# Performance work log

Measured on AMD Instinct MI355X. Metric: run time of the kernel, lower is better.

The kernel has to match this reference:

```python
import jax, jax.numpy as jnp
import numpy as np

N_DOMAINS = 8
LN_EPS = 1e-5


def setup_inputs() -> dict:
    key = jax.random.key(0)
    ks = jax.random.split(key, 4)
    N, D_IN, D_HID, D_OUT = 32768, 256, 1024, 256
    x = jax.random.normal(ks[0], (N, D_IN), dtype=jnp.float32)
    domain_types = jax.random.randint(ks[1], (N,), 0, N_DOMAINS, dtype=jnp.int32)
    # Per-domain MLP parameters (8 independent experts)
    W1 = jax.random.normal(ks[2], (N_DOMAINS, D_IN, D_HID), dtype=jnp.float32) * (1.0 / np.sqrt(D_IN))
    b1 = jnp.zeros((N_DOMAINS, D_HID), dtype=jnp.float32)
    gamma = jnp.ones((N_DOMAINS, D_HID), dtype=jnp.float32)
    beta = jnp.zeros((N_DOMAINS, D_HID), dtype=jnp.float32)
    W2 = jax.random.normal(ks[3], (N_DOMAINS, D_HID, D_OUT), dtype=jnp.float32) * (1.0 / np.sqrt(D_HID))
    b2 = jnp.zeros((N_DOMAINS, D_OUT), dtype=jnp.float32)
    return {"x": x, "domain_types": domain_types, "W1": W1, "b1": b1,
            "gamma": gamma, "beta": beta, "W2": W2, "b2": b2}


def _expert_mlp(x, W1d, b1d, gd, bd, W2d, b2d):
    # Linear -> LayerNorm -> ReLU -> (Dropout: identity at eval) -> Linear
    h = x @ W1d + b1d                       # [N, hid]
    mu = jnp.mean(h, axis=-1, keepdims=True)
    var = jnp.mean(jnp.square(h - mu), axis=-1, keepdims=True)
    h = (h - mu) * jax.lax.rsqrt(var + LN_EPS) * gd + bd
    h = jax.nn.relu(h)
    return h @ W2d + b2d                    # [N, out]


def reference(x, domain_types, W1, b1, gamma, beta, W2, b2):
    # output dim == x.shape[-1] (as in the torch code: zeros(batch, x.shape[-1]))
    out = jnp.zeros((x.shape[0], x.shape[-1]), dtype=x.dtype)
    for d in range(N_DOMAINS):  # small fixed expert loop (static MoE dispatch)
        y = _expert_mlp(x, W1[d], b1[d], gamma[d], beta[d], W2[d], b2[d])
        mask = (domain_types == d)[:, None]
        out = jnp.where(mask, y, out)
    return out
```

## Files before the change

kernel.cpp:

```cpp
#include <hip/hip_runtime.h>
#include <hip/hip_bf16.h>


#define ND 8
#define NROWS 32768
#define DIN 256
#define DHID 1024
#define DOUT 256
#define MPAD 33792
#define NTILES 264

typedef short short8 __attribute__((ext_vector_type(8)));
typedef unsigned short ushort8v __attribute__((ext_vector_type(8)));
typedef float floatx4 __attribute__((ext_vector_type(4)));

__device__ __forceinline__ unsigned short f2bf(float f) {
    unsigned u = __builtin_bit_cast(unsigned, f);
    unsigned r = u + 0x7fff + ((u >> 16) & 1);
    return (unsigned short)(r >> 16);
}
__device__ __forceinline__ float bf2f(unsigned short h) {
    unsigned u = ((unsigned)h) << 16;
    return __builtin_bit_cast(float, u);
}

#define GLDS16(gp, lp) __builtin_amdgcn_global_load_lds( \
    (const __attribute__((address_space(1))) void*)(gp), \
    (__attribute__((address_space(3))) void*)(lp), 16, 0, 0)

__global__ void transpose_histo(const float* __restrict__ W1,
                                const float* __restrict__ W2,
                                unsigned short* __restrict__ W1T,
                                unsigned short* __restrict__ W2T,
                                const int* __restrict__ dt,
                                int* __restrict__ counts) {
    const int z = blockIdx.z;
    if (z == 16) {
        const int bid = blockIdx.y * 8 + blockIdx.x;
        if (bid >= NROWS / 256) return;
        __shared__ int lc[ND];
        if (threadIdx.x < ND) lc[threadIdx.x] = 0;
        __syncthreads();
        atomicAdd(&lc[dt[bid * 256 + threadIdx.x]], 1);
        __syncthreads();
        if (threadIdx.x < ND) atomicAdd(&counts[threadIdx.x], lc[threadIdx.x]);
        return;
    }
    __shared__ float t[32][33];
    const bool isW1 = z < ND;
    const int d = isW1 ? z : z - ND;
    const int R = isW1 ? DIN : DHID;
    const int C = isW1 ? DHID : DOUT;
    const int r0 = (isW1 ? blockIdx.x : blockIdx.y) * 32;
    const int c0 = (isW1 ? blockIdx.y : blockIdx.x) * 32;
    const int tx = threadIdx.x & 31, ty = threadIdx.x >> 5;
    const float* src = (isW1 ? W1 : W2) + (size_t)d * R * C;
    unsigned short* dst = (isW1 ? W1T : W2T) + (size_t)d * R * C;
#pragma unroll
    for (int i = 0; i < 32; i += 8)
        t[ty + i][tx] = src[(size_t)(r0 + ty + i) * C + c0 + tx];
    __syncthreads();
#pragma unroll
    for (int i = 0; i < 32; i += 8)
        dst[(size_t)(c0 + ty + i) * R + r0 + tx] = f2bf(t[tx][ty + i]);
}

__global__ void make_meta(const int* __restrict__ counts, int* __restrict__ cursors,
                          int2* __restrict__ meta, int* __restrict__ perm) {
    __shared__ int ps[ND], pe[ND];
    if (threadIdx.x == 0) {
        int off = 0, t = 0;
        for (int d = 0; d < ND; d++) {
            cursors[d] = off;
            int nt = (counts[d] + 127) >> 7;
            for (int i = 0; i < nt; i++) meta[t++] = make_int2(d, off + (i << 7));
            ps[d] = off + counts[d];
            pe[d] = off + (nt << 7);
            off += nt << 7;
        }
        for (; t < NTILES; t++) meta[t] = make_int2(-1, 0);
    }
    __syncthreads();
#pragma unroll
    for (int d = 0; d < ND; d++)
        for (int p = ps[d] + threadIdx.x; p < pe[d]; p += 256) perm[p] = -1;
}

__global__ __launch_bounds__(256)
void assign_copy(const float* __restrict__ x, const int* __restrict__ dt,
                 int* __restrict__ cursors, int* __restrict__ perm,
                 unsigned short* __restrict__ xs) {
    __shared__ int lcnt[ND], lbase[ND];
    __shared__ int spos[256];
    const int tid = threadIdx.x;
    if (tid < ND) lcnt[tid] = 0;
    __syncthreads();
    const int r = blockIdx.x * 256 + tid;
    const int d = dt[r];
    const int myrank = atomicAdd(&lcnt[d], 1);
    __syncthreads();
    if (tid < ND && lcnt[tid] > 0)
        lbase[tid] = atomicAdd(&cursors[tid], lcnt[tid]);
    __syncthreads();
    const int p = lbase[d] + myrank;
    spos[tid] = p;
    perm[p] = r;
    __syncthreads();
    const int lane = tid & 63;
    const int sub = tid >> 6;
    for (int it = 0; it < 64; ++it) {
        const int lr = it * 4 + sub;
        const int gr = blockIdx.x * 256 + lr;
        const int pp = spos[lr];
        float4 v = ((const float4*)(x + (size_t)gr * DIN))[lane];
        ushort4 o;
        o.x = f2bf(v.x); o.y = f2bf(v.y); o.z = f2bf(v.z); o.w = f2bf(v.w);
        ((ushort4*)(xs + (size_t)pp * DIN))[lane] = o;
    }
}

__global__ __launch_bounds__(256, 2)
void gemm_a(const unsigned short* __restrict__ A,
            const unsigned short* __restrict__ Bt,
            const float* __restrict__ bias,
            const int2* __restrict__ meta,
            unsigned short* __restrict__ H,
            float2* __restrict__ stats) {
    const int2 md = meta[blockIdx.x];
    const int dom = md.x;
    if (dom < 0) return;
    const int m0 = md.y;
    const int n0 = blockIdx.y * 256;

    __shared__ unsigned short As[128 * 32];
    __shared__ unsigned short Bs[256 * 32];

    const int tid = threadIdx.x;
    const int lane = tid & 63;
    const int w = tid >> 6;
    const int wr = w >> 1, wc = w & 1;
    const int c16 = lane & 15, quad = lane >> 4;

    const unsigned short* Abase = A + (size_t)m0 * DIN;
    const unsigned short* Bbase = Bt + (size_t)dom * DHID * DIN + (size_t)n0 * DIN;

    floatx4 acc[4][8];
#pragma unroll
    for (int i = 0; i < 4; i++)
#pragma unroll
        for (int j = 0; j < 8; j++) acc[i][j] = 0.f;

    for (int k0 = 0; k0 < DIN; k0 += 32) {
#pragma unroll
        for (int it = 0; it < 2; ++it) {
            const int c = w * 128 + it * 64 + lane;
            const int m = c >> 2, kc = c & 3;
            GLDS16(Abase + (size_t)m * DIN + k0 + kc * 8, &As[(w * 128 + it * 64) * 8]);
        }
#pragma unroll
        for (int it = 0; it < 4; ++it) {
            const int c = w * 256 + it * 64 + lane;
            const int n = c >> 2, kc = c & 3;
            GLDS16(Bbase + (size_t)n * DIN + k0 + kc * 8, &Bs[(w * 256 + it * 64) * 8]);
        }
        __syncthreads();

        short8 a[4], b[8];
        const int kk = quad * 8;
#pragma unroll
        for (int i = 0; i < 4; i++)
            a[i] = *(const short8*)&As[(wr * 64 + i * 16 + c16) * 32 + kk];
#pragma unroll
        for (int j = 0; j < 8; j++)
            b[j] = *(const short8*)&Bs[(wc * 128 + j * 16 + c16) * 32 + kk];
#pragma unroll
        for (int i = 0; i < 4; i++)
#pragma unroll
            for (int j = 0; j < 8; j++)
                acc[i][j] = __builtin_amdgcn_mfma_f32_16x16x32_bf16(a[i], b[j], acc[i][j], 0, 0, 0);
        __syncthreads();
    }

    float bv[8];
#pragma unroll
    for (int j = 0; j < 8; j++)
        bv[j] = bias[dom * DHID + n0 + wc * 128 + j * 16 + c16];

    float2* st = stats + (size_t)(blockIdx.y * 2 + wc) * MPAD;
#pragma unroll
    for (int i = 0; i < 4; i++) {
        const int rowbase = m0 + wr * 64 + i * 16 + quad * 4;
#pragma unroll
        for (int r = 0; r < 4; r++) {
            float s = 0.f, q = 0.f;
            unsigned short* hrow = H + (size_t)(rowbase + r) * DHID + n0 + wc * 128;
#pragma unroll
            for (int j = 0; j < 8; j++) {
                const float v = acc[i][j][r] + bv[j];
                hrow[j * 16 + c16] = f2bf(v);
                s += v; q += v * v;
            }
#pragma unroll
            for (int o = 1; o < 16; o <<= 1) {
                s += __shfl_xor(s, o, 64);
                q += __shfl_xor(q, o, 64);
            }
            if (c16 == 0) st[rowbase + r] = make_float2(s, q);
        }
    }
}

__global__ __launch_bounds__(256)
void ln_relu(unsigned short* __restrict__ H,
             const float* __restrict__ gamma, const float* __restrict__ beta,
             const float2* __restrict__ stats, const int2* __restrict__ meta) {
    const int2 md = meta[blockIdx.x >> 2];
    const int dom = md.x;
    if (dom < 0) return;
    const int m0 = md.y + (blockIdx.x & 3) * 32;

    __shared__ float mu_s[32], rs_s[32];
    const int tid = threadIdx.x;
    if (tid < 32) {
        float s = 0.f, q = 0.f;
#pragma unroll
        for (int cb = 0; cb < 8; cb++) {
            const float2 p = stats[(size_t)cb * MPAD + m0 + tid];
            s += p.x; q += p.y;
        }
        const float inv = 1.0f / (float)DHID;
        const float mu = s * inv;
        const float var = fmaxf(q * inv - mu * mu, 0.f);
        mu_s[tid] = mu;
        rs_s[tid] = rsqrtf(var + 1e-5f);
    }
    const int cc = (tid & 127) * 8;
    const float4 g0 = *(const float4*)(gamma + dom * DHID + cc);
    const float4 g1 = *(const float4*)(gamma + dom * DHID + cc + 4);
    const float4 b0 = *(const float4*)(beta + dom * DHID + cc);
    const float4 b1 = *(const float4*)(beta + dom * DHID + cc + 4);
    const float gg[8] = {g0.x, g0.y, g0.z, g0.w, g1.x, g1.y, g1.z, g1.w};
    const float bb[8] = {b0.x, b0.y, b0.z, b0.w, b1.x, b1.y, b1.z, b1.w};
    __syncthreads();

    const int half = tid >> 7;
#pragma unroll 4
    for (int it = 0; it < 16; ++it) {
        const int lr = it * 2 + half;
        unsigned short* hp = H + (size_t)(m0 + lr) * DHID + cc;
        const ushort8v hv = *(const ushort8v*)hp;
        const float mu = mu_s[lr], rs = rs_s[lr];
        ushort8v o;
#pragma unroll
        for (int e = 0; e < 8; e++)
            o[e] = f2bf(fmaxf((bf2f(hv[e]) - mu) * rs * gg[e] + bb[e], 0.f));
        *(ushort8v*)hp = o;
    }
}

__global__ __launch_bounds__(256, 2)
void gemm_bt(const unsigned short* __restrict__ A,
             const unsigned short* __restrict__ Bt,
             const float* __restrict__ bias,
             const int2* __restrict__ meta,
             const int* __restrict__ perm,
             float* __restrict__ out) {
    const int2 md = meta[blockIdx.x];
    const int dom = md.x;
    if (dom < 0) return;
    const int m0 = md.y;
    const int n0 = blockIdx.y * 128;

    __shared__ unsigned short As[128 * 32];
    __shared__ unsigned short Bs[128 * 32];

    const int tid = threadIdx.x;
    const int lane = tid & 63;
    const int w = tid >> 6;
    const int wr = w >> 1, wc = w & 1;
    const int c16 = lane & 15, quad = lane >> 4;

    const unsigned short* Abase = A + (size_t)m0 * DHID;
    const unsigned short* Bbase = Bt + (size_t)dom * DOUT * DHID + (size_t)n0 * DHID;

    floatx4 acc[4][4];
#pragma unroll
    for (int i = 0; i < 4; i++)
#pragma unroll
        for (int j = 0; j < 4; j++) acc[i][j] = 0.f;

    for (int k0 = 0; k0 < DHID; k0 += 32) {
#pragma unroll
        for (int it = 0; it < 2; ++it) {
            const int c = w * 128 + it * 64 + lane;
            const int m = c >> 2, kc = c & 3;
            GLDS16(Abase + (size_t)m * DHID + k0 + kc * 8, &As[(w * 128 + it * 64) * 8]);
            GLDS16(Bbase + (size_t)m * DHID + k0 + kc * 8, &Bs[(w * 128 + it * 64) * 8]);
        }
        __syncthreads();

        short8 a[4], b[4];
        const int kk = quad * 8;
#pragma unroll
        for (int i = 0; i < 4; i++) {
            a[i] = *(const short8*)&As[(wr * 64 + i * 16 + c16) * 32 + kk];
            b[i] = *(const short8*)&Bs[(wc * 64 + i * 16 + c16) * 32 + kk];
        }
#pragma unroll
        for (int i = 0; i < 4; i++)
#pragma unroll
            for (int j = 0; j < 4; j++)
                acc[i][j] = __builtin_amdgcn_mfma_f32_16x16x32_bf16(a[i], b[j], acc[i][j], 0, 0, 0);
        __syncthreads();
    }

#pragma unroll
    for (int i = 0; i < 4; i++) {
        const int rowbase = m0 + wr * 64 + i * 16 + quad * 4;
#pragma unroll
        for (int r = 0; r < 4; r++) {
            const int orig = perm[rowbase + r];
            if (orig < 0) continue;
#pragma unroll
            for (int j = 0; j < 4; j++) {
                const int col = n0 + wc * 64 + j * 16 + c16;
                out[(size_t)orig * DOUT + col] = acc[i][j][r] + bias[dom * DOUT + col];
            }
        }
    }
}

extern "C" void kernel_launch(void* const* d_in, const int* in_sizes, int n_in,
                              void* d_out, int out_size, void* d_ws, size_t ws_size,
                              hipStream_t stream) {
    const float* x = (const float*)d_in[0];
    const int* dt = (const int*)d_in[1];
    const float* W1 = (const float*)d_in[2];
    const float* b1 = (const float*)d_in[3];
    const float* gamma = (const float*)d_in[4];
    const float* beta = (const float*)d_in[5];
    const float* W2 = (const float*)d_in[6];
    const float* b2 = (const float*)d_in[7];
    float* out = (float*)d_out;

    char* ws = (char*)d_ws;
    size_t off = 0;
    auto take = [&](size_t nbytes) -> char* {
        char* p = ws + off;
        off = (off + nbytes + 255) & ~(size_t)255;
        return p;
    };
    unsigned short* W1T = (unsigned short*)take((size_t)ND * DHID * DIN * 2);
    unsigned short* W2T = (unsigned short*)take((size_t)ND * DOUT * DHID * 2);
    unsigned short* XS  = (unsigned short*)take((size_t)MPAD * DIN * 2);
    unsigned short* H   = (unsigned short*)take((size_t)MPAD * DHID * 2);
    float2* STATS = (float2*)take((size_t)8 * MPAD * 8);
    int* PERM   = (int*)take(MPAD * 4);
    int* CNT    = (int*)take(64);
    int2* META  = (int2*)take(NTILES * 8);
    (void)ws_size; (void)n_in; (void)in_sizes; (void)out_size;

    int* COUNTS = CNT;
    int* CURSORS = CNT + 8;

    hipMemsetAsync(CNT, 0, 64, stream);
    transpose_histo<<<dim3(8, 32, 17), 256, 0, stream>>>(W1, W2, W1T, W2T, dt, COUNTS);
    make_meta<<<1, 256, 0, stream>>>(COUNTS, CURSORS, META, PERM);
    assign_copy<<<NROWS / 256, 256, 0, stream>>>(x, dt, CURSORS, PERM, XS);
    gemm_a<<<dim3(NTILES, 4), 256, 0, stream>>>(XS, W1T, b1, META, H, STATS);
    ln_relu<<<NTILES * 4, 256, 0, stream>>>(H, gamma, beta, STATS, META);
    gemm_bt<<<dim3(NTILES, 2), 256, 0, stream>>>(H, W2T, b2, META, PERM, out);
}
```

Baseline: 228.8 us.

## Use 256-row segments with 512-thread blocks for the first expert GEMM

```diff
diff --git a/kernel.cpp b/kernel.cpp
--- a/kernel.cpp
+++ b/kernel.cpp
@@ -7,8 +7,9 @@
 #define DIN 256
 #define DHID 1024
 #define DOUT 256
-#define MPAD 33792
-#define NTILES 264
+#define MPAD 34816
+#define NSEG 136
+#define NT128 272
 
 typedef short short8 __attribute__((ext_vector_type(8)));
 typedef unsigned short ushort8v __attribute__((ext_vector_type(8)));
@@ -66,19 +67,22 @@
 }
 
 __global__ void make_meta(const int* __restrict__ counts, int* __restrict__ cursors,
-                          int2* __restrict__ meta, int* __restrict__ perm) {
+                          int2* __restrict__ meta256, int2* __restrict__ meta128,
+                          int* __restrict__ perm) {
     __shared__ int ps[ND], pe[ND];
     if (threadIdx.x == 0) {
-        int off = 0, t = 0;
+        int off = 0, t2 = 0, t1 = 0;
         for (int d = 0; d < ND; d++) {
             cursors[d] = off;
-            int nt = (counts[d] + 127) >> 7;
-            for (int i = 0; i < nt; i++) meta[t++] = make_int2(d, off + (i << 7));
+            const int nt = (counts[d] + 255) >> 8;
+            for (int i = 0; i < nt; i++) meta256[t2++] = make_int2(d, off + (i << 8));
+            for (int i = 0; i < 2 * nt; i++) meta128[t1++] = make_int2(d, off + (i << 7));
             ps[d] = off + counts[d];
-            pe[d] = off + (nt << 7);
-            off += nt << 7;
-        }
-        for (; t < NTILES; t++) meta[t] = make_int2(-1, 0);
+            pe[d] = off + (nt << 8);
+            off = pe[d];
+        }
+        for (; t2 < NSEG; t2++) meta256[t2] = make_int2(-1, 0);
+        for (; t1 < NT128; t1++) meta128[t1] = make_int2(-1, 0);
     }
     __syncthreads();
 #pragma unroll
@@ -119,7 +123,7 @@
     }
 }
 
-__global__ __launch_bounds__(256, 2)
+__global__ __launch_bounds__(512, 4)
 void gemm_a(const unsigned short* __restrict__ A,
             const unsigned short* __restrict__ Bt,
             const float* __restrict__ bias,
@@ -132,7 +136,7 @@
     const int m0 = md.y;
     const int n0 = blockIdx.y * 256;
 
-    __shared__ unsigned short As[128 * 32];
+    __shared__ unsigned short As[256 * 32];
     __shared__ unsigned short Bs[256 * 32];
 
     const int tid = threadIdx.x;
@@ -158,10 +162,10 @@
             GLDS16(Abase + (size_t)m * DIN + k0 + kc * 8, &As[(w * 128 + it * 64) * 8]);
         }
 #pragma unroll
-        for (int it = 0; it < 4; ++it) {
-            const int c = w * 256 + it * 64 + lane;
+        for (int it = 0; it < 2; ++it) {
+            const int c = w * 128 + it * 64 + lane;
             const int n = c >> 2, kc = c & 3;
-            GLDS16(Bbase + (size_t)n * DIN + k0 + kc * 8, &Bs[(w * 256 + it * 64) * 8]);
+            GLDS16(Bbase + (size_t)n * DIN + k0 + kc * 8, &Bs[(w * 128 + it * 64) * 8]);
         }
         __syncthreads();
 
@@ -213,8 +217,8 @@
 __global__ __launch_bounds__(256)
 void ln_relu(unsigned short* __restrict__ H,
              const float* __restrict__ gamma, const float* __restrict__ beta,
-             const float2* __restrict__ stats, const int2* __restrict__ meta) {
-    const int2 md = meta[blockIdx.x >> 2];
+             const float2* __restrict__ stats, const int2* __restrict__ meta128) {
+    const int2 md = meta128[blockIdx.x >> 2];
     const int dom = md.x;
     if (dom < 0) return;
     const int m0 = md.y + (blockIdx.x & 3) * 32;
@@ -262,10 +266,10 @@
 void gemm_bt(const unsigned short* __restrict__ A,
              const unsigned short* __restrict__ Bt,
              const float* __restrict__ bias,
-             const int2* __restrict__ meta,
+             const int2* __restrict__ meta128,
              const int* __restrict__ perm,
              float* __restrict__ out) {
-    const int2 md = meta[blockIdx.x];
+    const int2 md = meta128[blockIdx.x];
     const int dom = md.x;
     if (dom < 0) return;
     const int m0 = md.y;
@@ -357,7 +361,8 @@
     float2* STATS = (float2*)take((size_t)8 * MPAD * 8);
     int* PERM   = (int*)take(MPAD * 4);
     int* CNT    = (int*)take(64);
-    int2* META  = (int2*)take(NTILES * 8);
+    int2* META256 = (int2*)take(NSEG * 8);
+    int2* META128 = (int2*)take(NT128 * 8);
     (void)ws_size; (void)n_in; (void)in_sizes; (void)out_size;
 
     int* COUNTS = CNT;
@@ -365,9 +370,9 @@
 
     hipMemsetAsync(CNT, 0, 64, stream);
     transpose_histo<<<dim3(8, 32, 17), 256, 0, stream>>>(W1, W2, W1T, W2T, dt, COUNTS);
-    make_meta<<<1, 256, 0, stream>>>(COUNTS, CURSORS, META, PERM);
+    make_meta<<<1, 256, 0, stream>>>(COUNTS, CURSORS, META256, META128, PERM);
     assign_copy<<<NROWS / 256, 256, 0, stream>>>(x, dt, CURSORS, PERM, XS);
-    gemm_a<<<dim3(NTILES, 4), 256, 0, stream>>>(XS, W1T, b1, META, H, STATS);
-    ln_relu<<<NTILES * 4, 256, 0, stream>>>(H, gamma, beta, STATS, META);
-    gemm_bt<<<dim3(NTILES, 2), 256, 0, stream>>>(H, W2T, b2, META, PERM, out);
-}
+    gemm_a<<<dim3(NSEG, 4), 512, 0, stream>>>(XS, W1T, b1, META256, H, STATS);
+    ln_relu<<<NT128 * 4, 256, 0, stream>>>(H, gamma, beta, STATS, META128);
+    gemm_bt<<<dim3(NT128, 2), 256, 0, stream>>>(H, W2T, b2, META128, PERM, out);
+}
```

New measurement: 420.5 us. 83.8% more time.
